# Performance work log

Measured on AMD Instinct MI355X. Metric: run time of the kernel, lower is better.

## Reference

```python
import jax, jax.numpy as jnp
import numpy as np
import math

B, N, D_IN, D = 64, 1024, 128, 128

def setup_inputs() -> dict:
    key = jax.random.key(0)
    ks = jax.random.split(key, 8)
    s_in = 1.0 / math.sqrt(D_IN)
    inp = {
        "x": jax.random.normal(ks[0], (B, N, D_IN), dtype=jnp.float32),
        "valid_lens": jax.random.randint(ks[1], (B,), 1, N + 1, dtype=jnp.int32),
        "Wq": jax.random.uniform(ks[2], (D_IN, D), jnp.float32, -s_in, s_in),
        "bq": jax.random.uniform(ks[3], (D,), jnp.float32, -s_in, s_in),
        "Wk": jax.random.uniform(ks[4], (D_IN, D), jnp.float32, -s_in, s_in),
        "bk": jax.random.uniform(ks[5], (D,), jnp.float32, -s_in, s_in),
        "Wv": jax.random.uniform(ks[6], (D_IN, D), jnp.float32, -s_in, s_in),
        "bv": jax.random.uniform(ks[7], (D,), jnp.float32, -s_in, s_in),
    }
    return inp

def reference(x, valid_lens, Wq, bq, Wk, bk, Wv, bv):
    # QKV projections
    q = x @ Wq + bq  # [B, N, D]
    k = x @ Wk + bk
    v = x @ Wv + bv
    scores = jnp.einsum("bnd,bmd->bnm", q, k) / math.sqrt(D)  # [B, N, N]
    # mask[b, i, j] = True where i >= valid_len[b] or j >= valid_len[b]
    idx = jnp.arange(N)
    invalid = idx[None, :] >= valid_lens[:, None]            # [B, N]
    mask = invalid[:, :, None] | invalid[:, None, :]          # [B, N, N]
    scores_masked = jnp.where(mask, jnp.float32(-1e12), scores)
    attn = jax.nn.softmax(scores_masked, axis=-1)
    attn = attn * (1.0 - mask.astype(attn.dtype))             # zero masked entries/rows
    return jnp.einsum("bnm,bmd->bnd", attn, v)
```

## Files before the change

kernel.cpp:

```cpp
#include <hip/hip_runtime.h>
#include <hip/hip_bf16.h>
#include <stdint.h>

#define B_ 64
#define N_ 1024
#define D_ 128

typedef __attribute__((ext_vector_type(8))) short bf16x8;
typedef __attribute__((ext_vector_type(4))) float f32x4;
typedef __attribute__((ext_vector_type(2))) unsigned int uint32x2;

__device__ __forceinline__ unsigned short f2bf(float f) {
    union { float f; uint32_t u; } v; v.f = f;
    uint32_t u = v.u;
    return (unsigned short)((u + 0x7FFFu + ((u >> 16) & 1u)) >> 16);
}

__global__ __launch_bounds__(256) void wtrans_kernel(
    const float* __restrict__ Wq, const float* __restrict__ Wk,
    const float* __restrict__ Wv, unsigned short* __restrict__ wt,
    int* __restrict__ ctr)
{
    if (blockIdx.x == 0 && threadIdx.x == 0) ctr[0] = 0;
    int p = blockIdx.x >> 4;
    int seg = blockIdx.x & 15;
    const float* W = (p == 0) ? Wq : (p == 1) ? Wk : Wv;
    unsigned short* dst = wt + p * (D_ * D_);
    for (int i = 0; i < 4; ++i) {
        int idx = seg * 1024 + i * 256 + (int)threadIdx.x;
        int k = idx >> 7, d = idx & 127;
        dst[d * D_ + k] = f2bf(W[idx]);
    }
}

__global__ __launch_bounds__(256) void proj_kernel(
    const float* __restrict__ x,
    const unsigned short* __restrict__ wtg,
    const float* __restrict__ bq, const float* __restrict__ bk,
    const float* __restrict__ bv,
    const int* __restrict__ valid_lens,
    unsigned short* __restrict__ qo, unsigned short* __restrict__ ko,
    unsigned short* __restrict__ vto)
{
    __shared__ alignas(16) unsigned short xs[64 * 136];
    __shared__ alignas(16) unsigned short ws[128 * 136];
    const int tid = threadIdx.x;
    const int row0 = blockIdx.x * 64;
    const int b = row0 >> 10, n0 = row0 & 1023;

    if (n0 >= valid_lens[b]) return;

    for (int it = 0; it < 8; ++it) {
        int idx4 = it * 256 + tid;
        int r = idx4 >> 5, c4 = (idx4 & 31) * 4;
        const float4 v = *(const float4*)&x[(size_t)(row0 + r) * D_ + c4];
        unsigned short tmp[4] = { f2bf(v.x), f2bf(v.y), f2bf(v.z), f2bf(v.w) };
        *(uint2*)&xs[r * 136 + c4] = *(uint2*)tmp;
    }

    const int wave = tid >> 6, lane = tid & 63;
    const int lr = lane & 15, lg = lane >> 4;
    const f32x4 zero4 = {0.f, 0.f, 0.f, 0.f};

    for (int p = 0; p < 3; ++p) {
        __syncthreads();
        const unsigned short* wsrc = wtg + p * (D_ * D_);
        for (int it = 0; it < 8; ++it) {
            int idx8 = it * 256 + tid;
            int r = idx8 >> 4, c8 = (idx8 & 15) * 8;
            *(bf16x8*)&ws[r * 136 + c8] = *(const bf16x8*)&wsrc[idx8 * 8];
        }
        __syncthreads();

        bf16x8 a[4];
        for (int kk = 0; kk < 4; ++kk)
            a[kk] = *(const bf16x8*)&xs[(wave * 16 + lr) * 136 + kk * 32 + lg * 8];
        f32x4 acc[8];
        for (int nt = 0; nt < 8; ++nt) acc[nt] = zero4;
        for (int kk = 0; kk < 4; ++kk)
            for (int nt = 0; nt < 8; ++nt) {
                bf16x8 bfr = *(const bf16x8*)&ws[(nt * 16 + lr) * 136 + kk * 32 + lg * 8];
                acc[nt] = __builtin_amdgcn_mfma_f32_16x16x32_bf16(a[kk], bfr, acc[nt], 0, 0, 0);
            }

        if (p < 2) {
            const float* bias = (p == 0) ? bq : bk;
            unsigned short* outp = (p == 0) ? qo : ko;
            const float sc = (p == 0) ? 0.12751741388f : 1.0f;
            __syncthreads();
            for (int nt = 0; nt < 8; ++nt) {
                int d = nt * 16 + lr;
                float bb = bias[d];
                for (int r = 0; r < 4; ++r)
                    ws[(wave * 16 + lg * 4 + r) * 136 + d] = f2bf((acc[nt][r] + bb) * sc);
            }
            __syncthreads();
            for (int it = 0; it < 4; ++it) {
                int idx = it * 256 + tid;
                int r = idx >> 4, c8 = (idx & 15) * 8;
                *(bf16x8*)&outp[(size_t)(row0 + r) * D_ + c8] =
                    *(const bf16x8*)&ws[r * 136 + c8];
            }
        } else {
            __syncthreads();
            for (int nt = 0; nt < 8; ++nt) {
                int d = nt * 16 + lr;
                float bb = bv[d];
                for (int r = 0; r < 4; ++r)
                    ws[d * 72 + wave * 16 + lg * 4 + r] = f2bf(acc[nt][r] + bb);
            }
            __syncthreads();
            unsigned short* dst = vto + ((size_t)b * D_) * N_ + n0;
            for (int it = 0; it < 4; ++it) {
                int idx = it * 256 + tid;
                int d = idx >> 3, c8 = (idx & 7) * 8;
                *(bf16x8*)&dst[(size_t)d * N_ + c8] = *(const bf16x8*)&ws[d * 72 + c8];
            }
        }
    }
}

__global__ __launch_bounds__(512, 1) void attn_kernel(
    const unsigned short* __restrict__ qg, const unsigned short* __restrict__ kg,
    const unsigned short* __restrict__ vtg, const int* __restrict__ valid_lens,
    float* __restrict__ out, int* __restrict__ ctr)
{
    __shared__ alignas(16) unsigned short smem[71680];
    __shared__ int slot;

    const int tid = threadIdx.x;
    const int wave = tid >> 6, lane = tid & 63;
    const int lr = lane & 15, lg = lane >> 4;
    const int grp = tid >> 8;
    const int wg = wave & 3;
    const int t256 = tid & 255;
    const int k_r = t256 >> 4, k_c = (t256 & 15) * 8;
    const int v_d = t256 >> 3, v_c = (t256 & 7) * 8;
    unsigned short* const ks_base = smem + grp * 17408;
    unsigned short* const vt_base = smem + 34816 + grp * 18432;
    float* const cmbF = (float*)smem;
    const f32x4 zero4 = {0.f, 0.f, 0.f, 0.f};
    const bool hbit = (lg >> 1) != 0;
    const bool mbit = (lg & 1) != 0;

    int item = blockIdx.x;
    while (item < 512) {
        const int qt = 7 - (item >> 6);
        const int b  = item & 63;
        const int L  = valid_lens[b];
        const int q0 = qt * 128;
        float* outb = out + ((size_t)b * N_ + q0) * D_;

        if (q0 >= L) {
            #pragma unroll
            for (int it = 0; it < 8; ++it) {
                int idx4 = it * 512 + tid;
                int r = idx4 >> 5, c4 = (idx4 & 31) * 4;
                float4 z; z.x = z.y = z.z = z.w = 0.f;
                *(float4*)&outb[(size_t)r * D_ + c4] = z;
            }
        } else {
            const int ntiles = (L + 63) >> 6;
            const int H = (ntiles + 1) >> 1;
            const int myStart = grp ? H : 0;
            const int myCnt = grp ? (ntiles - H) : H;
            const unsigned short* kgb = kg + (size_t)b * N_ * D_;
            const unsigned short* vtb = vtg + (size_t)b * D_ * N_;

            bf16x8 aq[2][4];
            #pragma unroll
            for (int rt = 0; rt < 2; ++rt) {
                const unsigned short* qrow =
                    qg + ((size_t)b * N_ + q0 + wg * 32 + rt * 16 + lr) * D_;
                #pragma unroll
                for (int kk = 0; kk < 4; ++kk)
                    aq[rt][kk] = *(const bf16x8*)&qrow[kk * 32 + lg * 8];
            }

            f32x4 oacc[2][8];
            #pragma unroll
            for (int rt = 0; rt < 2; ++rt)
                #pragma unroll
                for (int i = 0; i < 8; ++i) oacc[rt][i] = zero4;
            float lsum[2] = {0.f, 0.f};

            bf16x8 kreg[4], vreg[4];

            if (myCnt > 0) {
                const int kv0 = myStart * 64;
                #pragma unroll
                for (int it = 0; it < 4; ++it)
                    kreg[it] = *(const bf16x8*)&kgb[(size_t)(kv0 + it * 16 + k_r) * D_ + k_c];
                #pragma unroll
                for (int it = 0; it < 4; ++it)
                    vreg[it] = *(const bf16x8*)&vtb[(size_t)(it * 32 + v_d) * N_ + kv0 + v_c];
                #pragma unroll
                for (int it = 0; it < 4; ++it)
                    *(bf16x8*)&ks_base[(it * 16 + k_r) * 136 + k_c] = kreg[it];
                #pragma unroll
                for (int it = 0; it < 4; ++it)
                    *(bf16x8*)&vt_base[(it * 32 + v_d) * 72 + v_c] = vreg[it];
            }
            __syncthreads();

            for (int r = 0; r < H; ++r) {
                const bool valid = (r < myCnt);
                const int kv0 = (myStart + r) * 64;
                const int ko_cur = (r & 1) ? 8704 : 0;
                const int vo_cur = (r & 1) ? 9216 : 0;
                unsigned short* const ks_my = ks_base + ko_cur;
                unsigned short* const vt_my = vt_base + vo_cur;

                if (r + 1 < myCnt) {
                    const int kvn = kv0 + 64;
                    #pragma unroll
                    for (int it = 0; it < 4; ++it)
                        kreg[it] = *(const bf16x8*)&kgb[(size_t)(kvn + it * 16 + k_r) * D_ + k_c];
                    #pragma unroll
                    for (int it = 0; it < 4; ++it)
                        vreg[it] = *(const bf16x8*)&vtb[(size_t)(it * 32 + v_d) * N_ + kvn + v_c];
                    __builtin_amdgcn_sched_barrier(0);
                }

                if (valid) {
                    f32x4 s[2][4];
                    __builtin_amdgcn_s_setprio(1);
                    #pragma unroll
                    for (int nt = 0; nt < 4; ++nt) {
                        s[0][nt] = zero4; s[1][nt] = zero4;
                        #pragma unroll
                        for (int kk = 0; kk < 4; ++kk) {
                            bf16x8 bk_ = *(const bf16x8*)&ks_my[(nt * 16 + lr) * 136 + kk * 32 + lg * 8];
                            s[0][nt] = __builtin_amdgcn_mfma_f32_16x16x32_bf16(bk_, aq[0][kk], s[0][nt], 0, 0, 0);
                            s[1][nt] = __builtin_amdgcn_mfma_f32_16x16x32_bf16(bk_, aq[1][kk], s[1][nt], 0, 0, 0);
                        }
                    }
                    __builtin_amdgcn_s_setprio(0);

                    uint32_t pwv[2][8];
                    if (kv0 + 64 <= L) {
                        #pragma unroll
                        for (int nt = 0; nt < 4; ++nt)
                            #pragma unroll
                            for (int rt = 0; rt < 2; ++rt) {
                                float e0 = __builtin_amdgcn_exp2f(s[rt][nt][0]);
                                float e1 = __builtin_amdgcn_exp2f(s[rt][nt][1]);
                                float e2 = __builtin_amdgcn_exp2f(s[rt][nt][2]);
                                float e3 = __builtin_amdgcn_exp2f(s[rt][nt][3]);
                                lsum[rt] += (e0 + e1) + (e2 + e3);
                                uint32_t w0, w1;
                                asm("v_cvt_pk_bf16_f32 %0, %1, %2" : "=v"(w0) : "v"(e0), "v"(e1));
                                asm("v_cvt_pk_bf16_f32 %0, %1, %2" : "=v"(w1) : "v"(e2), "v"(e3));
                                pwv[rt][nt * 2 + 0] = w0;
                                pwv[rt][nt * 2 + 1] = w1;
                            }
                    } else {
                        #pragma unroll
                        for (int nt = 0; nt < 4; ++nt) {
                            const int kvb = kv0 + nt * 16 + lg * 4;
                            #pragma unroll
                            for (int rt = 0; rt < 2; ++rt) {
                                float e0 = (kvb + 0 < L) ? __builtin_amdgcn_exp2f(s[rt][nt][0]) : 0.f;
                                float e1 = (kvb + 1 < L) ? __builtin_amdgcn_exp2f(s[rt][nt][1]) : 0.f;
                                float e2 = (kvb + 2 < L) ? __builtin_amdgcn_exp2f(s[rt][nt][2]) : 0.f;
                                float e3 = (kvb + 3 < L) ? __builtin_amdgcn_exp2f(s[rt][nt][3]) : 0.f;
                                lsum[rt] += (e0 + e1) + (e2 + e3);
                                uint32_t w0, w1;
                                asm("v_cvt_pk_bf16_f32 %0, %1, %2" : "=v"(w0) : "v"(e0), "v"(e1));
                                asm("v_cvt_pk_bf16_f32 %0, %1, %2" : "=v"(w1) : "v"(e2), "v"(e3));
                                pwv[rt][nt * 2 + 0] = w0;
                                pwv[rt][nt * 2 + 1] = w1;
                            }
                        }
                    }

                    #pragma unroll
                    for (int rt = 0; rt < 2; ++rt) {
                        uint32_t sh[4], so[4];
                        #pragma unroll
                        for (int i = 0; i < 4; ++i) {
                            int i0 = (i >> 1) * 4 + (i & 1);
                            sh[i] = hbit ? pwv[rt][i0 + 2] : pwv[rt][i0];
                            so[i] = hbit ? pwv[rt][i0] : pwv[rt][i0 + 2];
                        }
                        uint32_t rv[4];
                        #pragma unroll
                        for (int i = 0; i < 4; ++i) {
#if __has_builtin(__builtin_amdgcn_permlane32_swap)
                            uint32x2 pr = __builtin_amdgcn_permlane32_swap(so[i], so[i], false, false);
                            rv[i] = hbit ? pr[0] : pr[1];
#else
                            rv[i] = (uint32_t)__shfl_xor((int)so[i], 32);
#endif
                        }
                        const bool c2 = (hbit != mbit);
                        uint32_t s2[4], kp[4];
                        #pragma unroll
                        for (int i = 0; i < 4; ++i) {
                            s2[i] = c2 ? sh[i] : rv[i];
                            kp[i] = c2 ? rv[i] : sh[i];
                        }
                        uint32_t r2v[4];
                        #pragma unroll
                        for (int i = 0; i < 4; ++i) {
#if __has_builtin(__builtin_amdgcn_permlane16_swap)
                            uint32x2 qr = __builtin_amdgcn_permlane16_swap(s2[i], s2[i], false, false);
                            r2v[i] = mbit ? qr[0] : qr[1];
#else
                            r2v[i] = (uint32_t)__shfl_xor((int)s2[i], 16);
#endif
                        }
                        uint32_t apw[2][4];
                        #pragma unroll
                        for (int kk = 0; kk < 2; ++kk)
                            #pragma unroll
                            for (int c = 0; c < 2; ++c) {
                                uint32_t kw = kp[kk * 2 + c], rw = r2v[kk * 2 + c];
                                apw[kk][c]     = mbit ? rw : kw;
                                apw[kk][2 + c] = mbit ? kw : rw;
                            }
                        __builtin_amdgcn_s_setprio(1);
                        #pragma unroll
                        for (int kk = 0; kk < 2; ++kk) {
                            bf16x8 ap = *(bf16x8*)&apw[kk][0];
                            #pragma unroll
                            for (int nt = 0; nt < 8; ++nt) {
                                bf16x8 bv_ = *(const bf16x8*)&vt_my[(nt * 16 + lr) * 72 + kk * 32 + lg * 8];
                                oacc[rt][nt] = __builtin_amdgcn_mfma_f32_16x16x32_bf16(ap, bv_, oacc[rt][nt], 0, 0, 0);
                            }
                        }
                        __builtin_amdgcn_s_setprio(0);
                    }
                }

                if (r + 1 < myCnt) {
                    unsigned short* const ks_nx = ks_base + (ko_cur ^ 8704);
                    unsigned short* const vt_nx = vt_base + (vo_cur ^ 9216);
                    #pragma unroll
                    for (int it = 0; it < 4; ++it)
                        *(bf16x8*)&ks_nx[(it * 16 + k_r) * 136 + k_c] = kreg[it];
                    #pragma unroll
                    for (int it = 0; it < 4; ++it)
                        *(bf16x8*)&vt_nx[(it * 32 + v_d) * 72 + v_c] = vreg[it];
                }
                __syncthreads();
            }

            #pragma unroll
            for (int rt = 0; rt < 2; ++rt) {
                float l = lsum[rt];
                l += __shfl_xor(l, 16);
                l += __shfl_xor(l, 32);
                lsum[rt] = l;
            }

            if (grp == 1) {
                #pragma unroll
                for (int rt = 0; rt < 2; ++rt) {
                    if (lg == 0) cmbF[17408 + wg * 32 + rt * 16 + lr] = lsum[rt];
                    #pragma unroll
                    for (int nt = 0; nt < 8; ++nt)
                        *(f32x4*)&cmbF[(t256 * 17 + rt * 8 + nt) * 4] = oacc[rt][nt];
                }
            }
            __syncthreads();
            if (grp == 0) {
                #pragma unroll
                for (int rt = 0; rt < 2; ++rt) {
                    const int qrow = q0 + wg * 32 + rt * 16 + lr;
                    float tot = lsum[rt] + cmbF[17408 + wg * 32 + rt * 16 + lr];
                    float invq = (qrow < L) ? 1.0f / tot : 0.0f;
                    f32x4 part[8];
                    #pragma unroll
                    for (int nt = 0; nt < 8; ++nt)
                        part[nt] = *(const f32x4*)&cmbF[(t256 * 17 + rt * 8 + nt) * 4];
                    #pragma unroll
                    for (int r2 = 0; r2 < 4; ++r2) {
                        const float invr = __shfl(invq, lg * 4 + r2);
                        const int row = wg * 32 + rt * 16 + lg * 4 + r2;
                        #pragma unroll
                        for (int nt = 0; nt < 8; ++nt) {
                            const int col = nt * 16 + lr;
                            outb[(size_t)row * D_ + col] =
                                (oacc[rt][nt][r2] + part[nt][r2]) * invr;
                        }
                    }
                }
            }
            __syncthreads();
        }

        if (tid == 0) slot = 256 + atomicAdd(ctr, 1);
        __syncthreads();
        item = slot;
        __syncthreads();
    }
}

extern "C" void kernel_launch(void* const* d_in, const int* in_sizes, int n_in,
                              void* d_out, int out_size, void* d_ws, size_t ws_size,
                              hipStream_t stream) {
    const float* x    = (const float*)d_in[0];
    const int*   vlen = (const int*)d_in[1];
    const float* Wq   = (const float*)d_in[2];
    const float* bq   = (const float*)d_in[3];
    const float* Wk   = (const float*)d_in[4];
    const float* bk   = (const float*)d_in[5];
    const float* Wv   = (const float*)d_in[6];
    const float* bv   = (const float*)d_in[7];
    float* out = (float*)d_out;

    unsigned short* wt  = (unsigned short*)d_ws;
    unsigned short* qws = (unsigned short*)((char*)d_ws + 98304);
    unsigned short* kws = qws + (size_t)B_ * N_ * D_;
    unsigned short* vtws = kws + (size_t)B_ * N_ * D_;
    int* ctr = (int*)((char*)d_ws + 98304 + 3 * (size_t)B_ * N_ * D_ * 2);

    wtrans_kernel<<<48, 256, 0, stream>>>(Wq, Wk, Wv, wt, ctr);
    proj_kernel<<<(B_ * N_) / 64, 256, 0, stream>>>(x, wt, bq, bk, bv, vlen, qws, kws, vtws);
    attn_kernel<<<256, 512, 0, stream>>>(qws, kws, vtws, vlen, out, ctr);
}
```

Baseline: 64.92 us.

## Fuse weight transpose, projection and attention into one persistent kernel with grid barriers

```diff
diff --git a/kernel.cpp b/kernel.cpp
--- a/kernel.cpp
+++ b/kernel.cpp
@@ -16,119 +16,141 @@
     return (unsigned short)((u + 0x7FFFu + ((u >> 16) & 1u)) >> 16);
 }
 
-__global__ __launch_bounds__(256) void wtrans_kernel(
-    const float* __restrict__ Wq, const float* __restrict__ Wk,
-    const float* __restrict__ Wv, unsigned short* __restrict__ wt,
-    int* __restrict__ ctr)
-{
-    if (blockIdx.x == 0 && threadIdx.x == 0) ctr[0] = 0;
-    int p = blockIdx.x >> 4;
-    int seg = blockIdx.x & 15;
-    const float* W = (p == 0) ? Wq : (p == 1) ? Wk : Wv;
-    unsigned short* dst = wt + p * (D_ * D_);
-    for (int i = 0; i < 4; ++i) {
-        int idx = seg * 1024 + i * 256 + (int)threadIdx.x;
-        int k = idx >> 7, d = idx & 127;
-        dst[d * D_ + k] = f2bf(W[idx]);
+__device__ __forceinline__ void gbar(int* c, int target) {
+    __syncthreads();
+    if (threadIdx.x == 0) {
+        __threadfence();
+        atomicAdd(c, 1);
+        while (atomicAdd(c, 0) < target) __builtin_amdgcn_s_sleep(2);
+        __threadfence();
     }
+    __syncthreads();
 }
 
-__global__ __launch_bounds__(256) void proj_kernel(
+__global__ __launch_bounds__(512, 1) void mega_kernel(
     const float* __restrict__ x,
-    const unsigned short* __restrict__ wtg,
-    const float* __restrict__ bq, const float* __restrict__ bk,
-    const float* __restrict__ bv,
+    const float* __restrict__ Wq, const float* __restrict__ bq,
+    const float* __restrict__ Wk, const float* __restrict__ bk,
+    const float* __restrict__ Wv, const float* __restrict__ bv,
     const int* __restrict__ valid_lens,
-    unsigned short* __restrict__ qo, unsigned short* __restrict__ ko,
-    unsigned short* __restrict__ vto)
-{
-    __shared__ alignas(16) unsigned short xs[64 * 136];
-    __shared__ alignas(16) unsigned short ws[128 * 136];
-    const int tid = threadIdx.x;
-    const int row0 = blockIdx.x * 64;
-    const int b = row0 >> 10, n0 = row0 & 1023;
-
-    if (n0 >= valid_lens[b]) return;
-
-    for (int it = 0; it < 8; ++it) {
-        int idx4 = it * 256 + tid;
-        int r = idx4 >> 5, c4 = (idx4 & 31) * 4;
-        const float4 v = *(const float4*)&x[(size_t)(row0 + r) * D_ + c4];
-        unsigned short tmp[4] = { f2bf(v.x), f2bf(v.y), f2bf(v.z), f2bf(v.w) };
-        *(uint2*)&xs[r * 136 + c4] = *(uint2*)tmp;
-    }
-
-    const int wave = tid >> 6, lane = tid & 63;
-    const int lr = lane & 15, lg = lane >> 4;
-    const f32x4 zero4 = {0.f, 0.f, 0.f, 0.f};
-
-    for (int p = 0; p < 3; ++p) {
-        __syncthreads();
-        const unsigned short* wsrc = wtg + p * (D_ * D_);
-        for (int it = 0; it < 8; ++it) {
-            int idx8 = it * 256 + tid;
-            int r = idx8 >> 4, c8 = (idx8 & 15) * 8;
-            *(bf16x8*)&ws[r * 136 + c8] = *(const bf16x8*)&wsrc[idx8 * 8];
-        }
-        __syncthreads();
-
-        bf16x8 a[4];
-        for (int kk = 0; kk < 4; ++kk)
-            a[kk] = *(const bf16x8*)&xs[(wave * 16 + lr) * 136 + kk * 32 + lg * 8];
-        f32x4 acc[8];
-        for (int nt = 0; nt < 8; ++nt) acc[nt] = zero4;
-        for (int kk = 0; kk < 4; ++kk)
-            for (int nt = 0; nt < 8; ++nt) {
-                bf16x8 bfr = *(const bf16x8*)&ws[(nt * 16 + lr) * 136 + kk * 32 + lg * 8];
-                acc[nt] = __builtin_amdgcn_mfma_f32_16x16x32_bf16(a[kk], bfr, acc[nt], 0, 0, 0);
-            }
-
-        if (p < 2) {
-            const float* bias = (p == 0) ? bq : bk;
-            unsigned short* outp = (p == 0) ? qo : ko;
-            const float sc = (p == 0) ? 0.12751741388f : 1.0f;
-            __syncthreads();
-            for (int nt = 0; nt < 8; ++nt) {
-                int d = nt * 16 + lr;
-                float bb = bias[d];
-                for (int r = 0; r < 4; ++r)
-                    ws[(wave * 16 + lg * 4 + r) * 136 + d] = f2bf((acc[nt][r] + bb) * sc);
-            }
-            __syncthreads();
-            for (int it = 0; it < 4; ++it) {
-                int idx = it * 256 + tid;
-                int r = idx >> 4, c8 = (idx & 15) * 8;
-                *(bf16x8*)&outp[(size_t)(row0 + r) * D_ + c8] =
-                    *(const bf16x8*)&ws[r * 136 + c8];
-            }
-        } else {
-            __syncthreads();
-            for (int nt = 0; nt < 8; ++nt) {
-                int d = nt * 16 + lr;
-                float bb = bv[d];
-                for (int r = 0; r < 4; ++r)
-                    ws[d * 72 + wave * 16 + lg * 4 + r] = f2bf(acc[nt][r] + bb);
-            }
-            __syncthreads();
-            unsigned short* dst = vto + ((size_t)b * D_) * N_ + n0;
-            for (int it = 0; it < 4; ++it) {
-                int idx = it * 256 + tid;
-                int d = idx >> 3, c8 = (idx & 7) * 8;
-                *(bf16x8*)&dst[(size_t)d * N_ + c8] = *(const bf16x8*)&ws[d * 72 + c8];
-            }
-        }
-    }
-}
-
-__global__ __launch_bounds__(512, 1) void attn_kernel(
-    const unsigned short* __restrict__ qg, const unsigned short* __restrict__ kg,
-    const unsigned short* __restrict__ vtg, const int* __restrict__ valid_lens,
+    unsigned short* __restrict__ wt,
+    unsigned short* __restrict__ qg, unsigned short* __restrict__ kg,
+    unsigned short* __restrict__ vtg,
     float* __restrict__ out, int* __restrict__ ctr)
 {
     __shared__ alignas(16) unsigned short smem[71680];
     __shared__ int slot;
 
     const int tid = threadIdx.x;
+    const f32x4 zero4 = {0.f, 0.f, 0.f, 0.f};
+
+    if (blockIdx.x < 48) {
+        int p = blockIdx.x >> 4, seg = blockIdx.x & 15;
+        const float* W = (p == 0) ? Wq : (p == 1) ? Wk : Wv;
+        unsigned short* dst = wt + p * (D_ * D_);
+        #pragma unroll
+        for (int i = 0; i < 2; ++i) {
+            int idx = seg * 1024 + i * 512 + tid;
+            int k = idx >> 7, d = idx & 127;
+            dst[d * D_ + k] = f2bf(W[idx]);
+        }
+    }
+    gbar(ctr + 1, 256);
+
+    {
+        const int half = tid >> 8, t256 = tid & 255;
+        unsigned short* const xs = smem + half * 26112;
+        unsigned short* const ws = smem + half * 26112 + 8704;
+        const int pwave = t256 >> 6, plane = t256 & 63;
+        const int lr = plane & 15, lg = plane >> 4;
+
+        for (int j = 0; j < 2; ++j) {
+            const int T = blockIdx.x + 256 * half + 512 * j;
+            const int row0 = T * 64;
+            const int b = T >> 4, n0 = row0 & 1023;
+            const bool act = (n0 < valid_lens[b]);
+
+            if (act) {
+                for (int it = 0; it < 8; ++it) {
+                    int idx4 = it * 256 + t256;
+                    int r = idx4 >> 5, c4 = (idx4 & 31) * 4;
+                    const float4 v = *(const float4*)&x[(size_t)(row0 + r) * D_ + c4];
+                    unsigned short tmp[4] = { f2bf(v.x), f2bf(v.y), f2bf(v.z), f2bf(v.w) };
+                    *(uint2*)&xs[r * 136 + c4] = *(uint2*)tmp;
+                }
+            }
+
+            for (int p = 0; p < 3; ++p) {
+                __syncthreads();
+                if (act) {
+                    const unsigned short* wsrc = wt + p * (D_ * D_);
+                    for (int it = 0; it < 8; ++it) {
+                        int idx8 = it * 256 + t256;
+                        int r = idx8 >> 4, c8 = (idx8 & 15) * 8;
+                        *(bf16x8*)&ws[r * 136 + c8] = *(const bf16x8*)&wsrc[idx8 * 8];
+                    }
+                }
+                __syncthreads();
+
+                f32x4 acc[8];
+                if (act) {
+                    bf16x8 a[4];
+                    for (int kk = 0; kk < 4; ++kk)
+                        a[kk] = *(const bf16x8*)&xs[(pwave * 16 + lr) * 136 + kk * 32 + lg * 8];
+                    for (int nt = 0; nt < 8; ++nt) acc[nt] = zero4;
+                    for (int kk = 0; kk < 4; ++kk)
+                        for (int nt = 0; nt < 8; ++nt) {
+                            bf16x8 bfr = *(const bf16x8*)&ws[(nt * 16 + lr) * 136 + kk * 32 + lg * 8];
+                            acc[nt] = __builtin_amdgcn_mfma_f32_16x16x32_bf16(a[kk], bfr, acc[nt], 0, 0, 0);
+                        }
+                }
+                __syncthreads();
+
+                if (p < 2) {
+                    if (act) {
+                        const float* bias = (p == 0) ? bq : bk;
+                        const float sc = (p == 0) ? 0.12751741388f : 1.0f;
+                        for (int nt = 0; nt < 8; ++nt) {
+                            int d = nt * 16 + lr;
+                            float bb = bias[d];
+                            for (int r = 0; r < 4; ++r)
+                                ws[(pwave * 16 + lg * 4 + r) * 136 + d] = f2bf((acc[nt][r] + bb) * sc);
+                        }
+                    }
+                    __syncthreads();
+                    if (act) {
+                        unsigned short* outp = (p == 0) ? qg : kg;
+                        for (int it = 0; it < 4; ++it) {
+                            int idx = it * 256 + t256;
+                            int r = idx >> 4, c8 = (idx & 15) * 8;
+                            *(bf16x8*)&outp[(size_t)(row0 + r) * D_ + c8] =
+                                *(const bf16x8*)&ws[r * 136 + c8];
+                        }
+                    }
+                } else {
+                    if (act) {
+                        for (int nt = 0; nt < 8; ++nt) {
+                            int d = nt * 16 + lr;
+                            float bb = bv[d];
+                            for (int r = 0; r < 4; ++r)
+                                ws[d * 72 + pwave * 16 + lg * 4 + r] = f2bf(acc[nt][r] + bb);
+                        }
+                    }
+                    __syncthreads();
+                    if (act) {
+                        unsigned short* dst = vtg + ((size_t)b * D_) * N_ + n0;
+                        for (int it = 0; it < 4; ++it) {
+                            int idx = it * 256 + t256;
+                            int d = idx >> 3, c8 = (idx & 7) * 8;
+                            *(bf16x8*)&dst[(size_t)d * N_ + c8] = *(const bf16x8*)&ws[d * 72 + c8];
+                        }
+                    }
+                }
+            }
+        }
+    }
+    gbar(ctr + 1, 512);
+
     const int wave = tid >> 6, lane = tid & 63;
     const int lr = lane & 15, lg = lane >> 4;
     const int grp = tid >> 8;
@@ -139,7 +161,6 @@
     unsigned short* const ks_base = smem + grp * 17408;
     unsigned short* const vt_base = smem + 34816 + grp * 18432;
     float* const cmbF = (float*)smem;
-    const f32x4 zero4 = {0.f, 0.f, 0.f, 0.f};
     const bool hbit = (lg >> 1) != 0;
     const bool mbit = (lg & 1) != 0;
 
@@ -416,7 +437,7 @@
     unsigned short* vtws = kws + (size_t)B_ * N_ * D_;
     int* ctr = (int*)((char*)d_ws + 98304 + 3 * (size_t)B_ * N_ * D_ * 2);
 
-    wtrans_kernel<<<48, 256, 0, stream>>>(Wq, Wk, Wv, wt, ctr);
-    proj_kernel<<<(B_ * N_) / 64, 256, 0, stream>>>(x, wt, bq, bk, bv, vlen, qws, kws, vtws);
-    attn_kernel<<<256, 512, 0, stream>>>(qws, kws, vtws, vlen, out, ctr);
+    hipMemsetAsync(ctr, 0, 8, stream);
+    mega_kernel<<<256, 512, 0, stream>>>(x, Wq, bq, Wk, bk, Wv, bv, vlen,
+                                         wt, qws, kws, vtws, out, ctr);
 }
```

Result: slower. 108.2 us (+66.7%).

## Replace persistent atomic work queue with one block per tile and single-buffered LDS

Applied to the files above, without the earlier changes.

```diff
diff --git a/kernel.cpp b/kernel.cpp
--- a/kernel.cpp
+++ b/kernel.cpp
@@ -18,10 +18,8 @@
 
 __global__ __launch_bounds__(256) void wtrans_kernel(
     const float* __restrict__ Wq, const float* __restrict__ Wk,
-    const float* __restrict__ Wv, unsigned short* __restrict__ wt,
-    int* __restrict__ ctr)
+    const float* __restrict__ Wv, unsigned short* __restrict__ wt)
 {
-    if (blockIdx.x == 0 && threadIdx.x == 0) ctr[0] = 0;
     int p = blockIdx.x >> 4;
     int seg = blockIdx.x & 15;
     const float* W = (p == 0) ? Wq : (p == 1) ? Wk : Wv;
@@ -120,13 +118,12 @@
     }
 }
 
-__global__ __launch_bounds__(512, 1) void attn_kernel(
+__global__ __launch_bounds__(512, 4) void attn_kernel(
     const unsigned short* __restrict__ qg, const unsigned short* __restrict__ kg,
     const unsigned short* __restrict__ vtg, const int* __restrict__ valid_lens,
-    float* __restrict__ out, int* __restrict__ ctr)
+    float* __restrict__ out)
 {
-    __shared__ alignas(16) unsigned short smem[71680];
-    __shared__ int slot;
+    __shared__ alignas(16) unsigned short smem[35840];
 
     const int tid = threadIdx.x;
     const int wave = tid >> 6, lane = tid & 63;
@@ -136,264 +133,252 @@
     const int t256 = tid & 255;
     const int k_r = t256 >> 4, k_c = (t256 & 15) * 8;
     const int v_d = t256 >> 3, v_c = (t256 & 7) * 8;
-    unsigned short* const ks_base = smem + grp * 17408;
-    unsigned short* const vt_base = smem + 34816 + grp * 18432;
+    unsigned short* const ks_my = smem + grp * 8704;
+    unsigned short* const vt_my = smem + 17408 + grp * 9216;
     float* const cmbF = (float*)smem;
     const f32x4 zero4 = {0.f, 0.f, 0.f, 0.f};
     const bool hbit = (lg >> 1) != 0;
     const bool mbit = (lg & 1) != 0;
 
-    int item = blockIdx.x;
-    while (item < 512) {
-        const int qt = 7 - (item >> 6);
-        const int b  = item & 63;
-        const int L  = valid_lens[b];
-        const int q0 = qt * 128;
-        float* outb = out + ((size_t)b * N_ + q0) * D_;
-
-        if (q0 >= L) {
-            #pragma unroll
-            for (int it = 0; it < 8; ++it) {
-                int idx4 = it * 512 + tid;
-                int r = idx4 >> 5, c4 = (idx4 & 31) * 4;
-                float4 z; z.x = z.y = z.z = z.w = 0.f;
-                *(float4*)&outb[(size_t)r * D_ + c4] = z;
-            }
-        } else {
-            const int ntiles = (L + 63) >> 6;
-            const int H = (ntiles + 1) >> 1;
-            const int myStart = grp ? H : 0;
-            const int myCnt = grp ? (ntiles - H) : H;
-            const unsigned short* kgb = kg + (size_t)b * N_ * D_;
-            const unsigned short* vtb = vtg + (size_t)b * D_ * N_;
-
-            bf16x8 aq[2][4];
-            #pragma unroll
-            for (int rt = 0; rt < 2; ++rt) {
-                const unsigned short* qrow =
-                    qg + ((size_t)b * N_ + q0 + wg * 32 + rt * 16 + lr) * D_;
-                #pragma unroll
-                for (int kk = 0; kk < 4; ++kk)
-                    aq[rt][kk] = *(const bf16x8*)&qrow[kk * 32 + lg * 8];
-            }
-
-            f32x4 oacc[2][8];
-            #pragma unroll
-            for (int rt = 0; rt < 2; ++rt)
-                #pragma unroll
-                for (int i = 0; i < 8; ++i) oacc[rt][i] = zero4;
-            float lsum[2] = {0.f, 0.f};
-
-            bf16x8 kreg[4], vreg[4];
-
-            if (myCnt > 0) {
-                const int kv0 = myStart * 64;
-                #pragma unroll
-                for (int it = 0; it < 4; ++it)
-                    kreg[it] = *(const bf16x8*)&kgb[(size_t)(kv0 + it * 16 + k_r) * D_ + k_c];
-                #pragma unroll
-                for (int it = 0; it < 4; ++it)
-                    vreg[it] = *(const bf16x8*)&vtb[(size_t)(it * 32 + v_d) * N_ + kv0 + v_c];
-                #pragma unroll
-                for (int it = 0; it < 4; ++it)
-                    *(bf16x8*)&ks_base[(it * 16 + k_r) * 136 + k_c] = kreg[it];
-                #pragma unroll
-                for (int it = 0; it < 4; ++it)
-                    *(bf16x8*)&vt_base[(it * 32 + v_d) * 72 + v_c] = vreg[it];
-            }
-            __syncthreads();
-
-            for (int r = 0; r < H; ++r) {
-                const bool valid = (r < myCnt);
-                const int kv0 = (myStart + r) * 64;
-                const int ko_cur = (r & 1) ? 8704 : 0;
-                const int vo_cur = (r & 1) ? 9216 : 0;
-                unsigned short* const ks_my = ks_base + ko_cur;
-                unsigned short* const vt_my = vt_base + vo_cur;
-
-                if (r + 1 < myCnt) {
-                    const int kvn = kv0 + 64;
-                    #pragma unroll
-                    for (int it = 0; it < 4; ++it)
-                        kreg[it] = *(const bf16x8*)&kgb[(size_t)(kvn + it * 16 + k_r) * D_ + k_c];
-                    #pragma unroll
-                    for (int it = 0; it < 4; ++it)
-                        vreg[it] = *(const bf16x8*)&vtb[(size_t)(it * 32 + v_d) * N_ + kvn + v_c];
-                    __builtin_amdgcn_sched_barrier(0);
-                }
-
-                if (valid) {
-                    f32x4 s[2][4];
-                    __builtin_amdgcn_s_setprio(1);
-                    #pragma unroll
-                    for (int nt = 0; nt < 4; ++nt) {
-                        s[0][nt] = zero4; s[1][nt] = zero4;
-                        #pragma unroll
-                        for (int kk = 0; kk < 4; ++kk) {
-                            bf16x8 bk_ = *(const bf16x8*)&ks_my[(nt * 16 + lr) * 136 + kk * 32 + lg * 8];
-                            s[0][nt] = __builtin_amdgcn_mfma_f32_16x16x32_bf16(bk_, aq[0][kk], s[0][nt], 0, 0, 0);
-                            s[1][nt] = __builtin_amdgcn_mfma_f32_16x16x32_bf16(bk_, aq[1][kk], s[1][nt], 0, 0, 0);
-                        }
-                    }
-                    __builtin_amdgcn_s_setprio(0);
-
-                    uint32_t pwv[2][8];
-                    if (kv0 + 64 <= L) {
-                        #pragma unroll
-                        for (int nt = 0; nt < 4; ++nt)
-                            #pragma unroll
-                            for (int rt = 0; rt < 2; ++rt) {
-                                float e0 = __builtin_amdgcn_exp2f(s[rt][nt][0]);
-                                float e1 = __builtin_amdgcn_exp2f(s[rt][nt][1]);
-                                float e2 = __builtin_amdgcn_exp2f(s[rt][nt][2]);
-                                float e3 = __builtin_amdgcn_exp2f(s[rt][nt][3]);
-                                lsum[rt] += (e0 + e1) + (e2 + e3);
-                                uint32_t w0, w1;
-                                asm("v_cvt_pk_bf16_f32 %0, %1, %2" : "=v"(w0) : "v"(e0), "v"(e1));
-                                asm("v_cvt_pk_bf16_f32 %0, %1, %2" : "=v"(w1) : "v"(e2), "v"(e3));
-                                pwv[rt][nt * 2 + 0] = w0;
-                                pwv[rt][nt * 2 + 1] = w1;
-                            }
-                    } else {
-                        #pragma unroll
-                        for (int nt = 0; nt < 4; ++nt) {
-                            const int kvb = kv0 + nt * 16 + lg * 4;
-                            #pragma unroll
-                            for (int rt = 0; rt < 2; ++rt) {
-                                float e0 = (kvb + 0 < L) ? __builtin_amdgcn_exp2f(s[rt][nt][0]) : 0.f;
-                                float e1 = (kvb + 1 < L) ? __builtin_amdgcn_exp2f(s[rt][nt][1]) : 0.f;
-                                float e2 = (kvb + 2 < L) ? __builtin_amdgcn_exp2f(s[rt][nt][2]) : 0.f;
-                                float e3 = (kvb + 3 < L) ? __builtin_amdgcn_exp2f(s[rt][nt][3]) : 0.f;
-                                lsum[rt] += (e0 + e1) + (e2 + e3);
-                                uint32_t w0, w1;
-                                asm("v_cvt_pk_bf16_f32 %0, %1, %2" : "=v"(w0) : "v"(e0), "v"(e1));
-                                asm("v_cvt_pk_bf16_f32 %0, %1, %2" : "=v"(w1) : "v"(e2), "v"(e3));
-                                pwv[rt][nt * 2 + 0] = w0;
-                                pwv[rt][nt * 2 + 1] = w1;
-                            }
-                        }
-                    }
-
+    const int id = blockIdx.x;
+    const int x_ = id & 7, g = id >> 3;
+    const int qt = g & 7;
+    const int b = ((g >> 3) << 3) + x_;
+    const int L = valid_lens[b];
+    const int q0 = qt * 128;
+    float* outb = out + ((size_t)b * N_ + q0) * D_;
+
+    if (q0 >= L) {
+        #pragma unroll
+        for (int it = 0; it < 8; ++it) {
+            int idx4 = it * 512 + tid;
+            int r = idx4 >> 5, c4 = (idx4 & 31) * 4;
+            float4 z; z.x = z.y = z.z = z.w = 0.f;
+            *(float4*)&outb[(size_t)r * D_ + c4] = z;
+        }
+        return;
+    }
+
+    const int ntiles = (L + 63) >> 6;
+    const int H = (ntiles + 1) >> 1;
+    const int myStart = grp ? H : 0;
+    const int myCnt = grp ? (ntiles - H) : H;
+    const unsigned short* kgb = kg + (size_t)b * N_ * D_;
+    const unsigned short* vtb = vtg + (size_t)b * D_ * N_;
+
+    bf16x8 aq[2][4];
+    #pragma unroll
+    for (int rt = 0; rt < 2; ++rt) {
+        const unsigned short* qrow =
+            qg + ((size_t)b * N_ + q0 + wg * 32 + rt * 16 + lr) * D_;
+        #pragma unroll
+        for (int kk = 0; kk < 4; ++kk)
+            aq[rt][kk] = *(const bf16x8*)&qrow[kk * 32 + lg * 8];
+    }
+
+    f32x4 oacc[2][8];
+    #pragma unroll
+    for (int rt = 0; rt < 2; ++rt)
+        #pragma unroll
+        for (int i = 0; i < 8; ++i) oacc[rt][i] = zero4;
+    float lsum[2] = {0.f, 0.f};
+
+    bf16x8 kreg[4], vreg[4];
+
+    if (myCnt > 0) {
+        const int kv0 = myStart * 64;
+        #pragma unroll
+        for (int it = 0; it < 4; ++it)
+            kreg[it] = *(const bf16x8*)&kgb[(size_t)(kv0 + it * 16 + k_r) * D_ + k_c];
+        #pragma unroll
+        for (int it = 0; it < 4; ++it)
+            vreg[it] = *(const bf16x8*)&vtb[(size_t)(it * 32 + v_d) * N_ + kv0 + v_c];
+        #pragma unroll
+        for (int it = 0; it < 4; ++it)
+            *(bf16x8*)&ks_my[(it * 16 + k_r) * 136 + k_c] = kreg[it];
+        #pragma unroll
+        for (int it = 0; it < 4; ++it)
+            *(bf16x8*)&vt_my[(it * 32 + v_d) * 72 + v_c] = vreg[it];
+    }
+    __syncthreads();
+
+    for (int r = 0; r < H; ++r) {
+        const bool valid = (r < myCnt);
+        const int kv0 = (myStart + r) * 64;
+
+        if (r + 1 < myCnt) {
+            const int kvn = kv0 + 64;
+            #pragma unroll
+            for (int it = 0; it < 4; ++it)
+                kreg[it] = *(const bf16x8*)&kgb[(size_t)(kvn + it * 16 + k_r) * D_ + k_c];
+            #pragma unroll
+            for (int it = 0; it < 4; ++it)
+                vreg[it] = *(const bf16x8*)&vtb[(size_t)(it * 32 + v_d) * N_ + kvn + v_c];
+            __builtin_amdgcn_sched_barrier(0);
+        }
+
+        if (valid) {
+            f32x4 s[2][4];
+            __builtin_amdgcn_s_setprio(1);
+            #pragma unroll
+            for (int nt = 0; nt < 4; ++nt) {
+                s[0][nt] = zero4; s[1][nt] = zero4;
+                #pragma unroll
+                for (int kk = 0; kk < 4; ++kk) {
+                    bf16x8 bk_ = *(const bf16x8*)&ks_my[(nt * 16 + lr) * 136 + kk * 32 + lg * 8];
+                    s[0][nt] = __builtin_amdgcn_mfma_f32_16x16x32_bf16(bk_, aq[0][kk], s[0][nt], 0, 0, 0);
+                    s[1][nt] = __builtin_amdgcn_mfma_f32_16x16x32_bf16(bk_, aq[1][kk], s[1][nt], 0, 0, 0);
+                }
+            }
+            __builtin_amdgcn_s_setprio(0);
+
+            uint32_t pwv[2][8];
+            if (kv0 + 64 <= L) {
+                #pragma unroll
+                for (int nt = 0; nt < 4; ++nt)
                     #pragma unroll
                     for (int rt = 0; rt < 2; ++rt) {
-                        uint32_t sh[4], so[4];
-                        #pragma unroll
-                        for (int i = 0; i < 4; ++i) {
-                            int i0 = (i >> 1) * 4 + (i & 1);
-                            sh[i] = hbit ? pwv[rt][i0 + 2] : pwv[rt][i0];
-                            so[i] = hbit ? pwv[rt][i0] : pwv[rt][i0 + 2];
-                        }
-                        uint32_t rv[4];
-                        #pragma unroll
-                        for (int i = 0; i < 4; ++i) {
+                        float e0 = __builtin_amdgcn_exp2f(s[rt][nt][0]);
+                        float e1 = __builtin_amdgcn_exp2f(s[rt][nt][1]);
+                        float e2 = __builtin_amdgcn_exp2f(s[rt][nt][2]);
+                        float e3 = __builtin_amdgcn_exp2f(s[rt][nt][3]);
+                        lsum[rt] += (e0 + e1) + (e2 + e3);
+                        uint32_t w0, w1;
+                        asm("v_cvt_pk_bf16_f32 %0, %1, %2" : "=v"(w0) : "v"(e0), "v"(e1));
+                        asm("v_cvt_pk_bf16_f32 %0, %1, %2" : "=v"(w1) : "v"(e2), "v"(e3));
+                        pwv[rt][nt * 2 + 0] = w0;
+                        pwv[rt][nt * 2 + 1] = w1;
+                    }
+            } else {
+                #pragma unroll
+                for (int nt = 0; nt < 4; ++nt) {
+                    const int kvb = kv0 + nt * 16 + lg * 4;
+                    #pragma unroll
+                    for (int rt = 0; rt < 2; ++rt) {
+                        float e0 = (kvb + 0 < L) ? __builtin_amdgcn_exp2f(s[rt][nt][0]) : 0.f;
+                        float e1 = (kvb + 1 < L) ? __builtin_amdgcn_exp2f(s[rt][nt][1]) : 0.f;
+                        float e2 = (kvb + 2 < L) ? __builtin_amdgcn_exp2f(s[rt][nt][2]) : 0.f;
+                        float e3 = (kvb + 3 < L) ? __builtin_amdgcn_exp2f(s[rt][nt][3]) : 0.f;
+                        lsum[rt] += (e0 + e1) + (e2 + e3);
+                        uint32_t w0, w1;
+                        asm("v_cvt_pk_bf16_f32 %0, %1, %2" : "=v"(w0) : "v"(e0), "v"(e1));
+                        asm("v_cvt_pk_bf16_f32 %0, %1, %2" : "=v"(w1) : "v"(e2), "v"(e3));
+                        pwv[rt][nt * 2 + 0] = w0;
+                        pwv[rt][nt * 2 + 1] = w1;
+                    }
+                }
+            }
+
+            #pragma unroll
+            for (int rt = 0; rt < 2; ++rt) {
+                uint32_t sh[4], so[4];
+                #pragma unroll
+                for (int i = 0; i < 4; ++i) {
+                    int i0 = (i >> 1) * 4 + (i & 1);
+                    sh[i] = hbit ? pwv[rt][i0 + 2] : pwv[rt][i0];
+                    so[i] = hbit ? pwv[rt][i0] : pwv[rt][i0 + 2];
+                }
+                uint32_t rv[4];
+                #pragma unroll
+                for (int i = 0; i < 4; ++i) {
 #if __has_builtin(__builtin_amdgcn_permlane32_swap)
-                            uint32x2 pr = __builtin_amdgcn_permlane32_swap(so[i], so[i], false, false);
-                            rv[i] = hbit ? pr[0] : pr[1];
+                    uint32x2 pr = __builtin_amdgcn_permlane32_swap(so[i], so[i], false, false);
+                    rv[i] = hbit ? pr[0] : pr[1];
 #else
-                            rv[i] = (uint32_t)__shfl_xor((int)so[i], 32);
+                    rv[i] = (uint32_t)__shfl_xor((int)so[i], 32);
 #endif
-                        }
-                        const bool c2 = (hbit != mbit);
-                        uint32_t s2[4], kp[4];
-                        #pragma unroll
-                        for (int i = 0; i < 4; ++i) {
-                            s2[i] = c2 ? sh[i] : rv[i];
-                            kp[i] = c2 ? rv[i] : sh[i];
-                        }
-                        uint32_t r2v[4];
-                        #pragma unroll
-                        for (int i = 0; i < 4; ++i) {
+                }
+                const bool c2 = (hbit != mbit);
+                uint32_t s2[4], kp[4];
+                #pragma unroll
+                for (int i = 0; i < 4; ++i) {
+                    s2[i] = c2 ? sh[i] : rv[i];
+                    kp[i] = c2 ? rv[i] : sh[i];
+                }
+                uint32_t r2v[4];
+                #pragma unroll
+                for (int i = 0; i < 4; ++i) {
 #if __has_builtin(__builtin_amdgcn_permlane16_swap)
-                            uint32x2 qr = __builtin_amdgcn_permlane16_swap(s2[i], s2[i], false, false);
-                            r2v[i] = mbit ? qr[0] : qr[1];
+                    uint32x2 qr = __builtin_amdgcn_permlane16_swap(s2[i], s2[i], false, false);
+                    r2v[i] = mbit ? qr[0] : qr[1];
 #else
-                            r2v[i] = (uint32_t)__shfl_xor((int)s2[i], 16);
+                    r2v[i] = (uint32_t)__shfl_xor((int)s2[i], 16);
 #endif
-                        }
-                        uint32_t apw[2][4];
-                        #pragma unroll
-                        for (int kk = 0; kk < 2; ++kk)
-                            #pragma unroll
-                            for (int c = 0; c < 2; ++c) {
-                                uint32_t kw = kp[kk * 2 + c], rw = r2v[kk * 2 + c];
-                                apw[kk][c]     = mbit ? rw : kw;
-                                apw[kk][2 + c] = mbit ? kw : rw;
-                            }
-                        __builtin_amdgcn_s_setprio(1);
-                        #pragma unroll
-                        for (int kk = 0; kk < 2; ++kk) {
-                            bf16x8 ap = *(bf16x8*)&apw[kk][0];
-                            #pragma unroll
-                            for (int nt = 0; nt < 8; ++nt) {
-                                bf16x8 bv_ = *(const bf16x8*)&vt_my[(nt * 16 + lr) * 72 + kk * 32 + lg * 8];
-                                oacc[rt][nt] = __builtin_amdgcn_mfma_f32_16x16x32_bf16(ap, bv_, oacc[rt][nt], 0, 0, 0);
-                            }
-                        }
-                        __builtin_amdgcn_s_setprio(0);
+                }
+                uint32_t apw[2][4];
+                #pragma unroll
+                for (int kk = 0; kk < 2; ++kk)
+                    #pragma unroll
+                    for (int c = 0; c < 2; ++c) {
+                        uint32_t kw = kp[kk * 2 + c], rw = r2v[kk * 2 + c];
+                        apw[kk][c]     = mbit ? rw : kw;
+                        apw[kk][2 + c] = mbit ? kw : rw;
                     }
-                }
-
-                if (r + 1 < myCnt) {
-                    unsigned short* const ks_nx = ks_base + (ko_cur ^ 8704);
-                    unsigned short* const vt_nx = vt_base + (vo_cur ^ 9216);
+                __builtin_amdgcn_s_setprio(1);
+                #pragma unroll
+                for (int kk = 0; kk < 2; ++kk) {
+                    bf16x8 ap = *(bf16x8*)&apw[kk][0];
                     #pragma unroll
-                    for (int it = 0; it < 4; ++it)
-                        *(bf16x8*)&ks_nx[(it * 16 + k_r) * 136 + k_c] = kreg[it];
-                    #pragma unroll
-                    for (int it = 0; it < 4; ++it)
-                        *(bf16x8*)&vt_nx[(it * 32 + v_d) * 72 + v_c] = vreg[it];
-                }
-                __syncthreads();
-            }
-
-            #pragma unroll
-            for (int rt = 0; rt < 2; ++rt) {
-                float l = lsum[rt];
-                l += __shfl_xor(l, 16);
-                l += __shfl_xor(l, 32);
-                lsum[rt] = l;
-            }
-
-            if (grp == 1) {
-                #pragma unroll
-                for (int rt = 0; rt < 2; ++rt) {
-                    if (lg == 0) cmbF[17408 + wg * 32 + rt * 16 + lr] = lsum[rt];
-                    #pragma unroll
-                    for (int nt = 0; nt < 8; ++nt)
-                        *(f32x4*)&cmbF[(t256 * 17 + rt * 8 + nt) * 4] = oacc[rt][nt];
-                }
-            }
-            __syncthreads();
-            if (grp == 0) {
-                #pragma unroll
-                for (int rt = 0; rt < 2; ++rt) {
-                    const int qrow = q0 + wg * 32 + rt * 16 + lr;
-                    float tot = lsum[rt] + cmbF[17408 + wg * 32 + rt * 16 + lr];
-                    float invq = (qrow < L) ? 1.0f / tot : 0.0f;
-                    f32x4 part[8];
-                    #pragma unroll
-                    for (int nt = 0; nt < 8; ++nt)
-                        part[nt] = *(const f32x4*)&cmbF[(t256 * 17 + rt * 8 + nt) * 4];
-                    #pragma unroll
-                    for (int r2 = 0; r2 < 4; ++r2) {
-                        const float invr = __shfl(invq, lg * 4 + r2);
-                        const int row = wg * 32 + rt * 16 + lg * 4 + r2;
-                        #pragma unroll
-                        for (int nt = 0; nt < 8; ++nt) {
-                            const int col = nt * 16 + lr;
-                            outb[(size_t)row * D_ + col] =
-                                (oacc[rt][nt][r2] + part[nt][r2]) * invr;
-                        }
+                    for (int nt = 0; nt < 8; ++nt) {
+                        bf16x8 bv_ = *(const bf16x8*)&vt_my[(nt * 16 + lr) * 72 + kk * 32 + lg * 8];
+                        oacc[rt][nt] = __builtin_amdgcn_mfma_f32_16x16x32_bf16(ap, bv_, oacc[rt][nt], 0, 0, 0);
                     }
                 }
-            }
-            __syncthreads();
-        }
-
-        if (tid == 0) slot = 256 + atomicAdd(ctr, 1);
+                __builtin_amdgcn_s_setprio(0);
+            }
+        }
         __syncthreads();
-        item = slot;
+        if (r + 1 < myCnt) {
+            #pragma unroll
+            for (int it = 0; it < 4; ++it)
+                *(bf16x8*)&ks_my[(it * 16 + k_r) * 136 + k_c] = kreg[it];
+            #pragma unroll
+            for (int it = 0; it < 4; ++it)
+                *(bf16x8*)&vt_my[(it * 32 + v_d) * 72 + v_c] = vreg[it];
+        }
         __syncthreads();
+    }
+
+    #pragma unroll
+    for (int rt = 0; rt < 2; ++rt) {
+        float l = lsum[rt];
+        l += __shfl_xor(l, 16);
+        l += __shfl_xor(l, 32);
+        lsum[rt] = l;
+    }
+
+    if (grp == 1) {
+        #pragma unroll
+        for (int rt = 0; rt < 2; ++rt) {
+            if (lg == 0) cmbF[17408 + wg * 32 + rt * 16 + lr] = lsum[rt];
+            #pragma unroll
+            for (int nt = 0; nt < 8; ++nt)
+                *(f32x4*)&cmbF[(t256 * 17 + rt * 8 + nt) * 4] = oacc[rt][nt];
+        }
+    }
+    __syncthreads();
+    if (grp == 0) {
+        #pragma unroll
+        for (int rt = 0; rt < 2; ++rt) {
+            const int qrow = q0 + wg * 32 + rt * 16 + lr;
+            float tot = lsum[rt] + cmbF[17408 + wg * 32 + rt * 16 + lr];
+            float invq = (qrow < L) ? 1.0f / tot : 0.0f;
+            f32x4 part[8];
+            #pragma unroll
+            for (int nt = 0; nt < 8; ++nt)
+                part[nt] = *(const f32x4*)&cmbF[(t256 * 17 + rt * 8 + nt) * 4];
+            #pragma unroll
+            for (int r2 = 0; r2 < 4; ++r2) {
+                const float invr = __shfl(invq, lg * 4 + r2);
+                const int row = wg * 32 + rt * 16 + lg * 4 + r2;
+                #pragma unroll
+                for (int nt = 0; nt < 8; ++nt) {
+                    const int col = nt * 16 + lr;
+                    outb[(size_t)row * D_ + col] =
+                        (oacc[rt][nt][r2] + part[nt][r2]) * invr;
+                }
+            }
+        }
     }
 }
 
@@ -414,9 +399,8 @@
     unsigned short* qws = (unsigned short*)((char*)d_ws + 98304);
     unsigned short* kws = qws + (size_t)B_ * N_ * D_;
     unsigned short* vtws = kws + (size_t)B_ * N_ * D_;
-    int* ctr = (int*)((char*)d_ws + 98304 + 3 * (size_t)B_ * N_ * D_ * 2);
-
-    wtrans_kernel<<<48, 256, 0, stream>>>(Wq, Wk, Wv, wt, ctr);
+
+    wtrans_kernel<<<48, 256, 0, stream>>>(Wq, Wk, Wv, wt);
     proj_kernel<<<(B_ * N_) / 64, 256, 0, stream>>>(x, wt, bq, bk, bv, vlen, qws, kws, vtws);
-    attn_kernel<<<256, 512, 0, stream>>>(qws, kws, vtws, vlen, out, ctr);
+    attn_kernel<<<512, 512, 0, stream>>>(qws, kws, vtws, vlen, out);
 }
```

Result: slower. 181.9 us (+180.2%).
